# Kernel tuning notes

Measured on AMD Instinct MI355X. Metric: run time of the kernel, lower is better.

The kernel has to match this reference:

```python
import jax, jax.numpy as jnp
import numpy as np

F = 256

def setup_inputs() -> dict:
    key = jax.random.key(0)
    ks = jax.random.split(key, 6)
    s = 1.0 / np.sqrt(F)
    x = jax.random.normal(ks[0], (16, 1024, F), dtype=jnp.float32)
    W_alpha = jax.random.uniform(ks[1], (F, F), minval=-s, maxval=s, dtype=jnp.float32)
    W_beta = jax.random.uniform(ks[2], (F, F), minval=-s, maxval=s, dtype=jnp.float32)
    W_unary = jax.random.uniform(ks[3], (F, F), minval=-s, maxval=s, dtype=jnp.float32)
    b_unary = jax.random.uniform(ks[4], (F,), minval=-s, maxval=s, dtype=jnp.float32)
    W_r = jax.random.uniform(ks[5], (F, F), minval=-s, maxval=s, dtype=jnp.float32)
    return {"x": x, "W_alpha": W_alpha, "W_beta": W_beta, "W_unary": W_unary, "b_unary": b_unary, "W_r": W_r}

def reference(x, W_alpha, W_beta, W_unary, b_unary, W_r):
    # x: [B, N, F]; torch Linear computes x @ W^T (+ b)
    B, N, _ = x.shape
    alpha = jnp.einsum('bnf,gf->bng', x, W_alpha)
    beta = jnp.einsum('bnf,gf->bng', x, W_beta)
    unary = jnp.einsum('bnf,gf->bng', x, W_unary) + b_unary
    # scores: alpha_i . beta_j, diagonal excluded (i == j skipped in loop)
    scores = jnp.einsum('bif,bjf->bij', alpha, beta)
    scores = scores * (1.0 - jnp.eye(N, dtype=x.dtype))
    att = jnp.einsum('bij,bjf->bif', scores, unary) / N
    out = jnp.einsum('bif,gf->big', att, W_r) + x
    return out
```

## Files before the change

### kernel.cpp

```cpp
#include <hip/hip_runtime.h>


typedef __bf16 bf16;
typedef float floatx4 __attribute__((ext_vector_type(4)));
typedef bf16 bf16x8 __attribute__((ext_vector_type(8)));
typedef bf16 bf16x4 __attribute__((ext_vector_type(4)));

constexpr int FD = 256;
constexpr int NB = 16;
constexpr int NN = 1024;
constexpr int RR = NB * NN;

__global__ __launch_bounds__(256) void cvt_x(const float* __restrict__ x, bf16* __restrict__ xb) {
    int i = (blockIdx.x * 256 + threadIdx.x) * 4;
    float4 v = *(const float4*)&x[i];
    bf16x4 o = { (bf16)v.x, (bf16)v.y, (bf16)v.z, (bf16)v.w };
    *(bf16x4*)&xb[i] = o;
}

__global__ __launch_bounds__(256) void cvt_w(const float* Wa, const float* Wb, const float* Wu, const float* Wr,
                                             bf16* Wab, bf16* Wbb, bf16* Wub, bf16* Wrb) {
    const float* src; bf16* dst;
    switch (blockIdx.y) {
        case 0: src = Wa; dst = Wab; break;
        case 1: src = Wb; dst = Wbb; break;
        case 2: src = Wu; dst = Wub; break;
        default: src = Wr; dst = Wrb; break;
    }
    int i = (blockIdx.x * 256 + threadIdx.x) * 4;
    float4 v = *(const float4*)&src[i];
    bf16x4 o = { (bf16)v.x, (bf16)v.y, (bf16)v.z, (bf16)v.w };
    *(bf16x4*)&dst[i] = o;
}

__global__ __launch_bounds__(256)
void proj_mfma(const bf16* __restrict__ A,
               const bf16* __restrict__ W0, const bf16* __restrict__ W1, const bf16* __restrict__ W2,
               bf16* __restrict__ O0, bf16* __restrict__ O1, bf16* __restrict__ O2,
               const float* __restrict__ bu)
{
    constexpr int BM = 128, BN = 64, BK = 32, LDK = 40;
    __shared__ bf16 As[BM][LDK];
    __shared__ bf16 Bs[3][BN][LDK];
    const int tid = threadIdx.x;
    const int wave = tid >> 6, lane = tid & 63;
    const int q = lane >> 4, l16 = lane & 15;
    const int bm = blockIdx.y * BM, bn = blockIdx.x * BN;
    const bf16* Wp[3] = { W0, W1, W2 };

    floatx4 acc[3][2][4] = {};

    for (int k0 = 0; k0 < FD; k0 += BK) {
        {
            int c = tid;
            int row = c >> 2, k8 = (c & 3) * 8;
            *(int4*)&As[row][k8] = *(const int4*)&A[(size_t)(bm + row) * FD + k0 + k8];
            c = tid + 256; row = c >> 2; k8 = (c & 3) * 8;
            *(int4*)&As[row][k8] = *(const int4*)&A[(size_t)(bm + row) * FD + k0 + k8];
        }
        #pragma unroll
        for (int w = 0; w < 3; w++) {
            int row = tid >> 2, k8 = (tid & 3) * 8;
            *(int4*)&Bs[w][row][k8] = *(const int4*)&Wp[w][(size_t)(bn + row) * FD + k0 + k8];
        }
        __syncthreads();
        bf16x8 af[2];
        #pragma unroll
        for (int mi = 0; mi < 2; mi++)
            af[mi] = *(const bf16x8*)&As[wave * 32 + mi * 16 + l16][q * 8];
        #pragma unroll
        for (int w = 0; w < 3; w++) {
            bf16x8 bq[4];
            #pragma unroll
            for (int nj = 0; nj < 4; nj++)
                bq[nj] = *(const bf16x8*)&Bs[w][nj * 16 + l16][q * 8];
            #pragma unroll
            for (int mi = 0; mi < 2; mi++)
                #pragma unroll
                for (int nj = 0; nj < 4; nj++)
                    acc[w][mi][nj] = __builtin_amdgcn_mfma_f32_16x16x32_bf16(af[mi], bq[nj], acc[w][mi][nj], 0, 0, 0);
        }
        __syncthreads();
    }

    bf16* Op[3] = { O0, O1, O2 };
    #pragma unroll
    for (int w = 0; w < 3; w++) {
        #pragma unroll
        for (int mi = 0; mi < 2; mi++)
            #pragma unroll
            for (int i = 0; i < 4; i++) {
                int m = bm + wave * 32 + mi * 16 + q * 4 + i;
                #pragma unroll
                for (int nj = 0; nj < 4; nj++) {
                    int n = bn + nj * 16 + l16;
                    float v = acc[w][mi][nj][i];
                    if (w == 2) v += bu[n];
                    Op[w][(size_t)m * FD + n] = (bf16)v;
                }
            }
    }
}

template<int MODE>
__global__ __launch_bounds__(256)
void gemm_nt_mfma(const bf16* __restrict__ A, const bf16* __restrict__ Bmat, void* __restrict__ Cout,
                  const float* __restrict__ dvec, const bf16* __restrict__ U,
                  const float* __restrict__ res, int batchB)
{
    constexpr int BM = 128, BN = 64, BK = 32, LDK = 40;
    __shared__ bf16 As[BM][LDK];
    __shared__ bf16 Bs[BN][LDK];
    const int tid = threadIdx.x;
    const int wave = tid >> 6, lane = tid & 63;
    const int q = lane >> 4, l16 = lane & 15;
    const int bm = blockIdx.y * BM, bn = blockIdx.x * BN;
    const bf16* Bp = Bmat + (batchB ? (size_t)(bm >> 10) * FD * FD : 0);

    floatx4 acc[2][4] = {};

    for (int k0 = 0; k0 < FD; k0 += BK) {
        {
            int c = tid;
            int row = c >> 2, k8 = (c & 3) * 8;
            *(int4*)&As[row][k8] = *(const int4*)&A[(size_t)(bm + row) * FD + k0 + k8];
            c = tid + 256; row = c >> 2; k8 = (c & 3) * 8;
            *(int4*)&As[row][k8] = *(const int4*)&A[(size_t)(bm + row) * FD + k0 + k8];
            int rb = tid >> 2, kb8 = (tid & 3) * 8;
            *(int4*)&Bs[rb][kb8] = *(const int4*)&Bp[(size_t)(bn + rb) * FD + k0 + kb8];
        }
        __syncthreads();
        bf16x8 af[2], bq[4];
        #pragma unroll
        for (int mi = 0; mi < 2; mi++)
            af[mi] = *(const bf16x8*)&As[wave * 32 + mi * 16 + l16][q * 8];
        #pragma unroll
        for (int nj = 0; nj < 4; nj++)
            bq[nj] = *(const bf16x8*)&Bs[nj * 16 + l16][q * 8];
        #pragma unroll
        for (int mi = 0; mi < 2; mi++)
            #pragma unroll
            for (int nj = 0; nj < 4; nj++)
                acc[mi][nj] = __builtin_amdgcn_mfma_f32_16x16x32_bf16(af[mi], bq[nj], acc[mi][nj], 0, 0, 0);
        __syncthreads();
    }

    #pragma unroll
    for (int mi = 0; mi < 2; mi++)
        #pragma unroll
        for (int i = 0; i < 4; i++) {
            int m = bm + wave * 32 + mi * 16 + q * 4 + i;
            float dm = (MODE == 2) ? dvec[m] : 0.0f;
            #pragma unroll
            for (int nj = 0; nj < 4; nj++) {
                int n = bn + nj * 16 + l16;
                float v = acc[mi][nj][i];
                if (MODE == 2) {
                    v = (v - dm * (float)U[(size_t)m * FD + n]) * (1.0f / 1024.0f);
                    ((bf16*)Cout)[(size_t)m * FD + n] = (bf16)v;
                } else if (MODE == 3) {
                    ((float*)Cout)[(size_t)m * FD + n] = v + res[(size_t)m * FD + n];
                } else {
                    ((bf16*)Cout)[(size_t)m * FD + n] = (bf16)v;
                }
            }
        }
}

__global__ __launch_bounds__(256)
void gemm_tn_mfma(const bf16* __restrict__ Uall, const bf16* __restrict__ Ball, float* __restrict__ Mpart)
{
    constexpr int BG = 64, BF = 64, BK = 32, LDK = 40, CHUNK = 256;
    __shared__ bf16 Ags[BG][LDK];
    __shared__ bf16 Bfs[BF][LDK];
    const int tid = threadIdx.x;
    const int wave = tid >> 6, lane = tid & 63;
    const int q = lane >> 4, l16 = lane & 15;
    const int b = blockIdx.z >> 2, chunk = blockIdx.z & 3;
    const int bg = blockIdx.y * BG, bfo = blockIdx.x * BF;
    const bf16* Ub = Uall + (size_t)b * NN * FD;
    const bf16* Bt = Ball + (size_t)b * NN * FD;

    floatx4 acc[4] = {};

    const int n0base = chunk * CHUNK;
    for (int nc = 0; nc < CHUNK; nc += BK) {
        {
            int nr = tid >> 3, g8 = (tid & 7) * 8;
            bf16x8 va = *(const bf16x8*)&Ub[(size_t)(n0base + nc + nr) * FD + bg + g8];
            bf16x8 vb = *(const bf16x8*)&Bt[(size_t)(n0base + nc + nr) * FD + bfo + g8];
            #pragma unroll
            for (int j = 0; j < 8; j++) {
                Ags[g8 + j][nr] = va[j];
                Bfs[g8 + j][nr] = vb[j];
            }
        }
        __syncthreads();
        bf16x8 af = *(const bf16x8*)&Ags[wave * 16 + l16][q * 8];
        #pragma unroll
        for (int fj = 0; fj < 4; fj++) {
            bf16x8 bq = *(const bf16x8*)&Bfs[fj * 16 + l16][q * 8];
            acc[fj] = __builtin_amdgcn_mfma_f32_16x16x32_bf16(af, bq, acc[fj], 0, 0, 0);
        }
        __syncthreads();
    }

    float* P = Mpart + (size_t)chunk * (NB * FD * FD) + (size_t)b * FD * FD;
    #pragma unroll
    for (int i = 0; i < 4; i++) {
        int g = bg + wave * 16 + q * 4 + i;
        #pragma unroll
        for (int fj = 0; fj < 4; fj++) {
            int f = bfo + fj * 16 + l16;
            P[(size_t)g * FD + f] = acc[fj][i];
        }
    }
}

__global__ __launch_bounds__(256) void reduce_M(const float* __restrict__ Mpart, bf16* __restrict__ Mt) {
    int i = (blockIdx.x * 256 + threadIdx.x) * 4;
    const size_t S = (size_t)NB * FD * FD;
    float4 a = *(const float4*)&Mpart[i];
    float4 c = *(const float4*)&Mpart[S + i];
    float4 e = *(const float4*)&Mpart[2 * S + i];
    float4 g = *(const float4*)&Mpart[3 * S + i];
    bf16x4 o = { (bf16)(a.x + c.x + e.x + g.x), (bf16)(a.y + c.y + e.y + g.y),
                 (bf16)(a.z + c.z + e.z + g.z), (bf16)(a.w + c.w + e.w + g.w) };
    *(bf16x4*)&Mt[i] = o;
}

__global__ __launch_bounds__(256)
void d_dot(const bf16* __restrict__ alpha, const bf16* __restrict__ beta, float* __restrict__ d) {
    const int row = blockIdx.x * 4 + (threadIdx.x >> 6);
    const int lane = threadIdx.x & 63;
    const size_t base = (size_t)row * FD;
    bf16x4 av = *(const bf16x4*)&alpha[base + lane * 4];
    bf16x4 bv = *(const bf16x4*)&beta[base + lane * 4];
    float s = (float)av[0] * (float)bv[0] + (float)av[1] * (float)bv[1] +
              (float)av[2] * (float)bv[2] + (float)av[3] * (float)bv[3];
    #pragma unroll
    for (int off = 32; off; off >>= 1) s += __shfl_xor(s, off);
    if (lane == 0) d[row] = s;
}

extern "C" void kernel_launch(void* const* d_in, const int* in_sizes, int n_in,
                              void* d_out, int out_size, void* d_ws, size_t ws_size,
                              hipStream_t stream)
{
    const float* x  = (const float*)d_in[0];
    const float* Wa = (const float*)d_in[1];
    const float* Wb = (const float*)d_in[2];
    const float* Wu = (const float*)d_in[3];
    const float* bu = (const float*)d_in[4];
    const float* Wr = (const float*)d_in[5];
    float* out = (float*)d_out;

    char* w = (char*)d_ws;
    bf16* xb    = (bf16*)w;                 w += (size_t)RR * FD * 2;
    bf16* Wab   = (bf16*)w;                 w += (size_t)FD * FD * 2;
    bf16* Wbb   = (bf16*)w;                 w += (size_t)FD * FD * 2;
    bf16* Wub   = (bf16*)w;                 w += (size_t)FD * FD * 2;
    bf16* Wrb   = (bf16*)w;                 w += (size_t)FD * FD * 2;
    bf16* alpha = (bf16*)w;                 w += (size_t)RR * FD * 2;
    bf16* beta  = (bf16*)w;                 w += (size_t)RR * FD * 2;
    bf16* unary = (bf16*)w;                 w += (size_t)RR * FD * 2;
    bf16* Tb    = (bf16*)w;                 w += (size_t)RR * FD * 2;
    float* dv   = (float*)w;                w += (size_t)RR * 4;
    float* Mpart= (float*)w;                w += (size_t)4 * NB * FD * FD * 4;
    bf16* Mt    = (bf16*)w;                 w += (size_t)NB * FD * FD * 2;

    dim3 blk(256);

    cvt_x<<<dim3(RR * FD / 1024), blk, 0, stream>>>(x, xb);
    cvt_w<<<dim3(FD * FD / 1024, 4), blk, 0, stream>>>(Wa, Wb, Wu, Wr, Wab, Wbb, Wub, Wrb);

    proj_mfma<<<dim3(FD / 64, RR / 128), blk, 0, stream>>>(xb, Wab, Wbb, Wub, alpha, beta, unary, bu);

    d_dot<<<dim3(RR / 4), blk, 0, stream>>>(alpha, beta, dv);

    gemm_tn_mfma<<<dim3(FD / 64, FD / 64, NB * 4), blk, 0, stream>>>(unary, beta, Mpart);
    reduce_M<<<dim3(NB * FD * FD / 1024), blk, 0, stream>>>(Mpart, Mt);

    gemm_nt_mfma<2><<<dim3(FD / 64, RR / 128), blk, 0, stream>>>(alpha, Mt, Tb, dv, unary, nullptr, 1);

    gemm_nt_mfma<3><<<dim3(FD / 64, RR / 128), blk, 0, stream>>>(Tb, Wrb, out, nullptr, nullptr, x, 0);
}
```

Before: 150.8 us.

## Fold output projection into per-batch matrix and fuse diagonal dot into projection

Reassociates the computation so that W_r is folded into the per-batch (beta^T unary) matrix, giving one small batched GEMM (qt_mfma). This removes the separate full-size output GEMM and the intermediate T buffer. The unary projection is pre-multiplied by W_r as a fourth projection (Wc = W_r·W_u, plus bias Wr·bu) inside the projection kernel. The diagonal alpha·beta dot is computed from the projection accumulators, and the weight conversions are merged into a single prep kernel along with the partial-sum reduction folded into qt_mfma. This cuts several launches and one large GEMM pass over activations. The cost is an extra 256-wide projection, a serial scalar prep for the Wc product, and additional bf16 rounding from reassociation.

```diff
diff --git a/kernel.cpp b/kernel.cpp
--- a/kernel.cpp
+++ b/kernel.cpp
@@ -11,55 +11,78 @@
 constexpr int NN = 1024;
 constexpr int RR = NB * NN;
 
-__global__ __launch_bounds__(256) void cvt_x(const float* __restrict__ x, bf16* __restrict__ xb) {
-    int i = (blockIdx.x * 256 + threadIdx.x) * 4;
-    float4 v = *(const float4*)&x[i];
-    bf16x4 o = { (bf16)v.x, (bf16)v.y, (bf16)v.z, (bf16)v.w };
-    *(bf16x4*)&xb[i] = o;
-}
-
-__global__ __launch_bounds__(256) void cvt_w(const float* Wa, const float* Wb, const float* Wu, const float* Wr,
-                                             bf16* Wab, bf16* Wbb, bf16* Wub, bf16* Wrb) {
-    const float* src; bf16* dst;
-    switch (blockIdx.y) {
-        case 0: src = Wa; dst = Wab; break;
-        case 1: src = Wb; dst = Wbb; break;
-        case 2: src = Wu; dst = Wub; break;
-        default: src = Wr; dst = Wrb; break;
-    }
-    int i = (blockIdx.x * 256 + threadIdx.x) * 4;
-    float4 v = *(const float4*)&src[i];
-    bf16x4 o = { (bf16)v.x, (bf16)v.y, (bf16)v.z, (bf16)v.w };
-    *(bf16x4*)&dst[i] = o;
-}
-
-__global__ __launch_bounds__(256)
-void proj_mfma(const bf16* __restrict__ A,
-               const bf16* __restrict__ W0, const bf16* __restrict__ W1, const bf16* __restrict__ W2,
-               bf16* __restrict__ O0, bf16* __restrict__ O1, bf16* __restrict__ O2,
-               const float* __restrict__ bu)
+__global__ __launch_bounds__(256)
+void prep(const float* __restrict__ x, const float* __restrict__ Wa, const float* __restrict__ Wb,
+          const float* __restrict__ Wu, const float* __restrict__ bu, const float* __restrict__ Wr,
+          bf16* __restrict__ xb, bf16* __restrict__ Wab, bf16* __restrict__ Wbb,
+          bf16* __restrict__ Wub, bf16* __restrict__ Wrb, bf16* __restrict__ Wcb,
+          float* __restrict__ bc)
+{
+    const int blk = blockIdx.x, tid = threadIdx.x;
+    if (blk < 2048) {
+        size_t i = ((size_t)blk * 256 + tid) * 8;
+        float4 v0 = *(const float4*)&x[i];
+        float4 v1 = *(const float4*)&x[i + 4];
+        bf16x8 o = { (bf16)v0.x, (bf16)v0.y, (bf16)v0.z, (bf16)v0.w,
+                     (bf16)v1.x, (bf16)v1.y, (bf16)v1.z, (bf16)v1.w };
+        *(bf16x8*)&xb[i] = o;
+    } else if (blk < 2080) {
+        int rel = blk - 2048, w = rel >> 3, wb = rel & 7;
+        const float* src = (w == 0) ? Wa : (w == 1) ? Wb : (w == 2) ? Wu : Wr;
+        bf16* dst = (w == 0) ? Wab : (w == 1) ? Wbb : (w == 2) ? Wub : Wrb;
+        for (int it = 0; it < 8; it++) {
+            int i = wb * 8192 + it * 1024 + tid * 4;
+            float4 v = *(const float4*)&src[i];
+            bf16x4 o = { (bf16)v.x, (bf16)v.y, (bf16)v.z, (bf16)v.w };
+            *(bf16x4*)&dst[i] = o;
+        }
+    } else if (blk < 2144) {
+        int j0 = (blk - 2080) * 4;
+        float acc[4] = {};
+        for (int g = 0; g < FD; g++) {
+            float wu = Wu[g * FD + tid];
+            #pragma unroll
+            for (int jr = 0; jr < 4; jr++)
+                acc[jr] += Wr[(j0 + jr) * FD + g] * wu;
+        }
+        #pragma unroll
+        for (int jr = 0; jr < 4; jr++)
+            Wcb[(j0 + jr) * FD + tid] = (bf16)acc[jr];
+    } else {
+        float s = 0.0f;
+        for (int g = 0; g < FD; g++) s += Wr[tid * FD + g] * bu[g];
+        bc[tid] = s;
+    }
+}
+
+__global__ __launch_bounds__(256)
+void proj4(const bf16* __restrict__ A,
+           const bf16* __restrict__ W0, const bf16* __restrict__ W1,
+           const bf16* __restrict__ W2, const bf16* __restrict__ W3,
+           bf16* __restrict__ O0, bf16* __restrict__ O1, bf16* __restrict__ O2, bf16* __restrict__ O3,
+           const float* __restrict__ bu, const float* __restrict__ bc,
+           float* __restrict__ dpart)
 {
     constexpr int BM = 128, BN = 64, BK = 32, LDK = 40;
     __shared__ bf16 As[BM][LDK];
-    __shared__ bf16 Bs[3][BN][LDK];
+    __shared__ bf16 Bs[4][BN][LDK];
     const int tid = threadIdx.x;
     const int wave = tid >> 6, lane = tid & 63;
     const int q = lane >> 4, l16 = lane & 15;
     const int bm = blockIdx.y * BM, bn = blockIdx.x * BN;
-    const bf16* Wp[3] = { W0, W1, W2 };
-
-    floatx4 acc[3][2][4] = {};
+    const bf16* Wp[4] = { W0, W1, W2, W3 };
+
+    floatx4 acc[4][2][4] = {};
 
     for (int k0 = 0; k0 < FD; k0 += BK) {
         {
-            int c = tid;
-            int row = c >> 2, k8 = (c & 3) * 8;
+            int c = tid, row = c >> 2, k8 = (c & 3) * 8;
             *(int4*)&As[row][k8] = *(const int4*)&A[(size_t)(bm + row) * FD + k0 + k8];
             c = tid + 256; row = c >> 2; k8 = (c & 3) * 8;
             *(int4*)&As[row][k8] = *(const int4*)&A[(size_t)(bm + row) * FD + k0 + k8];
         }
         #pragma unroll
-        for (int w = 0; w < 3; w++) {
+        for (int w = 0; w < 4; w++) {
             int row = tid >> 2, k8 = (tid & 3) * 8;
             *(int4*)&Bs[w][row][k8] = *(const int4*)&Wp[w][(size_t)(bn + row) * FD + k0 + k8];
         }
@@ -69,7 +92,7 @@
         for (int mi = 0; mi < 2; mi++)
             af[mi] = *(const bf16x8*)&As[wave * 32 + mi * 16 + l16][q * 8];
         #pragma unroll
-        for (int w = 0; w < 3; w++) {
+        for (int w = 0; w < 4; w++) {
             bf16x8 bq[4];
             #pragma unroll
             for (int nj = 0; nj < 4; nj++)
@@ -83,9 +106,9 @@
         __syncthreads();
     }
 
-    bf16* Op[3] = { O0, O1, O2 };
-    #pragma unroll
-    for (int w = 0; w < 3; w++) {
+    bf16* Op[4] = { O0, O1, O2, O3 };
+    #pragma unroll
+    for (int w = 0; w < 4; w++) {
         #pragma unroll
         for (int mi = 0; mi < 2; mi++)
             #pragma unroll
@@ -96,79 +119,31 @@
                     int n = bn + nj * 16 + l16;
                     float v = acc[w][mi][nj][i];
                     if (w == 2) v += bu[n];
+                    if (w == 3) v += bc[n];
                     Op[w][(size_t)m * FD + n] = (bf16)v;
                 }
             }
     }
-}
-
-template<int MODE>
-__global__ __launch_bounds__(256)
-void gemm_nt_mfma(const bf16* __restrict__ A, const bf16* __restrict__ Bmat, void* __restrict__ Cout,
-                  const float* __restrict__ dvec, const bf16* __restrict__ U,
-                  const float* __restrict__ res, int batchB)
-{
-    constexpr int BM = 128, BN = 64, BK = 32, LDK = 40;
-    __shared__ bf16 As[BM][LDK];
-    __shared__ bf16 Bs[BN][LDK];
-    const int tid = threadIdx.x;
-    const int wave = tid >> 6, lane = tid & 63;
-    const int q = lane >> 4, l16 = lane & 15;
-    const int bm = blockIdx.y * BM, bn = blockIdx.x * BN;
-    const bf16* Bp = Bmat + (batchB ? (size_t)(bm >> 10) * FD * FD : 0);
-
-    floatx4 acc[2][4] = {};
-
-    for (int k0 = 0; k0 < FD; k0 += BK) {
-        {
-            int c = tid;
-            int row = c >> 2, k8 = (c & 3) * 8;
-            *(int4*)&As[row][k8] = *(const int4*)&A[(size_t)(bm + row) * FD + k0 + k8];
-            c = tid + 256; row = c >> 2; k8 = (c & 3) * 8;
-            *(int4*)&As[row][k8] = *(const int4*)&A[(size_t)(bm + row) * FD + k0 + k8];
-            int rb = tid >> 2, kb8 = (tid & 3) * 8;
-            *(int4*)&Bs[rb][kb8] = *(const int4*)&Bp[(size_t)(bn + rb) * FD + k0 + kb8];
-        }
-        __syncthreads();
-        bf16x8 af[2], bq[4];
-        #pragma unroll
-        for (int mi = 0; mi < 2; mi++)
-            af[mi] = *(const bf16x8*)&As[wave * 32 + mi * 16 + l16][q * 8];
-        #pragma unroll
-        for (int nj = 0; nj < 4; nj++)
-            bq[nj] = *(const bf16x8*)&Bs[nj * 16 + l16][q * 8];
-        #pragma unroll
-        for (int mi = 0; mi < 2; mi++)
+
+    #pragma unroll
+    for (int mi = 0; mi < 2; mi++)
+        #pragma unroll
+        for (int i = 0; i < 4; i++) {
+            float p = 0.0f;
             #pragma unroll
             for (int nj = 0; nj < 4; nj++)
-                acc[mi][nj] = __builtin_amdgcn_mfma_f32_16x16x32_bf16(af[mi], bq[nj], acc[mi][nj], 0, 0, 0);
-        __syncthreads();
-    }
-
-    #pragma unroll
-    for (int mi = 0; mi < 2; mi++)
-        #pragma unroll
-        for (int i = 0; i < 4; i++) {
-            int m = bm + wave * 32 + mi * 16 + q * 4 + i;
-            float dm = (MODE == 2) ? dvec[m] : 0.0f;
-            #pragma unroll
-            for (int nj = 0; nj < 4; nj++) {
-                int n = bn + nj * 16 + l16;
-                float v = acc[mi][nj][i];
-                if (MODE == 2) {
-                    v = (v - dm * (float)U[(size_t)m * FD + n]) * (1.0f / 1024.0f);
-                    ((bf16*)Cout)[(size_t)m * FD + n] = (bf16)v;
-                } else if (MODE == 3) {
-                    ((float*)Cout)[(size_t)m * FD + n] = v + res[(size_t)m * FD + n];
-                } else {
-                    ((bf16*)Cout)[(size_t)m * FD + n] = (bf16)v;
-                }
+                p += acc[0][mi][nj][i] * acc[1][mi][nj][i];
+            #pragma unroll
+            for (int off = 1; off < 16; off <<= 1) p += __shfl_xor(p, off);
+            if (l16 == 0) {
+                int m = bm + wave * 32 + mi * 16 + q * 4 + i;
+                dpart[(size_t)blockIdx.x * RR + m] = p;
             }
         }
 }
 
 __global__ __launch_bounds__(256)
-void gemm_tn_mfma(const bf16* __restrict__ Uall, const bf16* __restrict__ Ball, float* __restrict__ Mpart)
+void gemm_tn_mfma(const bf16* __restrict__ Aall, const bf16* __restrict__ Ball, float* __restrict__ Mpart)
 {
     constexpr int BG = 64, BF = 64, BK = 32, LDK = 40, CHUNK = 256;
     __shared__ bf16 Ags[BG][LDK];
@@ -178,22 +153,19 @@
     const int q = lane >> 4, l16 = lane & 15;
     const int b = blockIdx.z >> 2, chunk = blockIdx.z & 3;
     const int bg = blockIdx.y * BG, bfo = blockIdx.x * BF;
-    const bf16* Ub = Uall + (size_t)b * NN * FD;
-    const bf16* Bt = Ball + (size_t)b * NN * FD;
+    const bf16* Ab = Aall + (size_t)b * NN * FD;
+    const bf16* Bb = Ball + (size_t)b * NN * FD;
 
     floatx4 acc[4] = {};
-
     const int n0base = chunk * CHUNK;
     for (int nc = 0; nc < CHUNK; nc += BK) {
-        {
-            int nr = tid >> 3, g8 = (tid & 7) * 8;
-            bf16x8 va = *(const bf16x8*)&Ub[(size_t)(n0base + nc + nr) * FD + bg + g8];
-            bf16x8 vb = *(const bf16x8*)&Bt[(size_t)(n0base + nc + nr) * FD + bfo + g8];
-            #pragma unroll
-            for (int j = 0; j < 8; j++) {
-                Ags[g8 + j][nr] = va[j];
-                Bfs[g8 + j][nr] = vb[j];
-            }
+        int nr = tid >> 3, g8 = (tid & 7) * 8;
+        bf16x8 va = *(const bf16x8*)&Ab[(size_t)(n0base + nc + nr) * FD + bg + g8];
+        bf16x8 vb = *(const bf16x8*)&Bb[(size_t)(n0base + nc + nr) * FD + bfo + g8];
+        #pragma unroll
+        for (int j = 0; j < 8; j++) {
+            Ags[g8 + j][nr] = va[j];
+            Bfs[g8 + j][nr] = vb[j];
         }
         __syncthreads();
         bf16x8 af = *(const bf16x8*)&Ags[wave * 16 + l16][q * 8];
@@ -204,43 +176,114 @@
         }
         __syncthreads();
     }
-
     float* P = Mpart + (size_t)chunk * (NB * FD * FD) + (size_t)b * FD * FD;
     #pragma unroll
     for (int i = 0; i < 4; i++) {
         int g = bg + wave * 16 + q * 4 + i;
         #pragma unroll
-        for (int fj = 0; fj < 4; fj++) {
-            int f = bfo + fj * 16 + l16;
-            P[(size_t)g * FD + f] = acc[fj][i];
-        }
-    }
-}
-
-__global__ __launch_bounds__(256) void reduce_M(const float* __restrict__ Mpart, bf16* __restrict__ Mt) {
-    int i = (blockIdx.x * 256 + threadIdx.x) * 4;
+        for (int fj = 0; fj < 4; fj++)
+            P[(size_t)g * FD + bfo + fj * 16 + l16] = acc[fj][i];
+    }
+}
+
+__global__ __launch_bounds__(256)
+void qt_mfma(const bf16* __restrict__ Wrb, const float* __restrict__ Mpart, bf16* __restrict__ Qt)
+{
+    constexpr int BJ = 64, BKT = 64, BK = 32, LDK = 40;
+    __shared__ bf16 As[BJ][LDK];
+    __shared__ bf16 Bs[BKT][LDK];
+    const int tid = threadIdx.x;
+    const int wave = tid >> 6, lane = tid & 63;
+    const int q = lane >> 4, l16 = lane & 15;
+    const int b = blockIdx.z;
+    const int bj = blockIdx.y * BJ, bk = blockIdx.x * BKT;
     const size_t S = (size_t)NB * FD * FD;
-    float4 a = *(const float4*)&Mpart[i];
-    float4 c = *(const float4*)&Mpart[S + i];
-    float4 e = *(const float4*)&Mpart[2 * S + i];
-    float4 g = *(const float4*)&Mpart[3 * S + i];
-    bf16x4 o = { (bf16)(a.x + c.x + e.x + g.x), (bf16)(a.y + c.y + e.y + g.y),
-                 (bf16)(a.z + c.z + e.z + g.z), (bf16)(a.w + c.w + e.w + g.w) };
-    *(bf16x4*)&Mt[i] = o;
-}
-
-__global__ __launch_bounds__(256)
-void d_dot(const bf16* __restrict__ alpha, const bf16* __restrict__ beta, float* __restrict__ d) {
-    const int row = blockIdx.x * 4 + (threadIdx.x >> 6);
-    const int lane = threadIdx.x & 63;
-    const size_t base = (size_t)row * FD;
-    bf16x4 av = *(const bf16x4*)&alpha[base + lane * 4];
-    bf16x4 bv = *(const bf16x4*)&beta[base + lane * 4];
-    float s = (float)av[0] * (float)bv[0] + (float)av[1] * (float)bv[1] +
-              (float)av[2] * (float)bv[2] + (float)av[3] * (float)bv[3];
-    #pragma unroll
-    for (int off = 32; off; off >>= 1) s += __shfl_xor(s, off);
-    if (lane == 0) d[row] = s;
+    const float* Mb = Mpart + (size_t)b * FD * FD;
+
+    floatx4 acc[4] = {};
+    for (int n0 = 0; n0 < FD; n0 += BK) {
+        int row = tid >> 2, n8 = (tid & 3) * 8;
+        *(int4*)&As[row][n8] = *(const int4*)&Wrb[(size_t)(bj + row) * FD + n0 + n8];
+        const float* base = &Mb[(size_t)(bk + row) * FD + n0 + n8];
+        float4 s0 = *(const float4*)&base[0]       , s1 = *(const float4*)&base[4];
+        float4 t0 = *(const float4*)&base[S]       , t1 = *(const float4*)&base[S + 4];
+        float4 u0 = *(const float4*)&base[2 * S]   , u1 = *(const float4*)&base[2 * S + 4];
+        float4 v0 = *(const float4*)&base[3 * S]   , v1 = *(const float4*)&base[3 * S + 4];
+        bf16x8 o = { (bf16)(s0.x + t0.x + u0.x + v0.x), (bf16)(s0.y + t0.y + u0.y + v0.y),
+                     (bf16)(s0.z + t0.z + u0.z + v0.z), (bf16)(s0.w + t0.w + u0.w + v0.w),
+                     (bf16)(s1.x + t1.x + u1.x + v1.x), (bf16)(s1.y + t1.y + u1.y + v1.y),
+                     (bf16)(s1.z + t1.z + u1.z + v1.z), (bf16)(s1.w + t1.w + u1.w + v1.w) };
+        *(bf16x8*)&Bs[row][n8] = o;
+        __syncthreads();
+        bf16x8 af = *(const bf16x8*)&As[wave * 16 + l16][q * 8];
+        #pragma unroll
+        for (int kj = 0; kj < 4; kj++) {
+            bf16x8 bq = *(const bf16x8*)&Bs[kj * 16 + l16][q * 8];
+            acc[kj] = __builtin_amdgcn_mfma_f32_16x16x32_bf16(af, bq, acc[kj], 0, 0, 0);
+        }
+        __syncthreads();
+    }
+    bf16* Qb = Qt + (size_t)b * FD * FD;
+    #pragma unroll
+    for (int i = 0; i < 4; i++) {
+        int j = bj + wave * 16 + q * 4 + i;
+        #pragma unroll
+        for (int kj = 0; kj < 4; kj++)
+            Qb[(size_t)j * FD + bk + kj * 16 + l16] = (bf16)acc[kj][i];
+    }
+}
+
+__global__ __launch_bounds__(256)
+void final_mfma(const bf16* __restrict__ alpha, const bf16* __restrict__ Qt,
+                const float* __restrict__ dpart, const bf16* __restrict__ U2,
+                const float* __restrict__ x, float* __restrict__ out)
+{
+    constexpr int BM = 128, BN = 64, BK = 32, LDK = 40;
+    __shared__ bf16 As[BM][LDK];
+    __shared__ bf16 Bs[BN][LDK];
+    const int tid = threadIdx.x;
+    const int wave = tid >> 6, lane = tid & 63;
+    const int q = lane >> 4, l16 = lane & 15;
+    const int bm = blockIdx.y * BM, bn = blockIdx.x * BN;
+    const bf16* Qb = Qt + (size_t)(bm >> 10) * FD * FD;
+
+    floatx4 acc[2][4] = {};
+    for (int k0 = 0; k0 < FD; k0 += BK) {
+        int c = tid, row = c >> 2, k8 = (c & 3) * 8;
+        *(int4*)&As[row][k8] = *(const int4*)&alpha[(size_t)(bm + row) * FD + k0 + k8];
+        c = tid + 256; row = c >> 2; k8 = (c & 3) * 8;
+        *(int4*)&As[row][k8] = *(const int4*)&alpha[(size_t)(bm + row) * FD + k0 + k8];
+        int rb = tid >> 2, kb8 = (tid & 3) * 8;
+        *(int4*)&Bs[rb][kb8] = *(const int4*)&Qb[(size_t)(bn + rb) * FD + k0 + kb8];
+        __syncthreads();
+        bf16x8 af[2], bq[4];
+        #pragma unroll
+        for (int mi = 0; mi < 2; mi++)
+            af[mi] = *(const bf16x8*)&As[wave * 32 + mi * 16 + l16][q * 8];
+        #pragma unroll
+        for (int nj = 0; nj < 4; nj++)
+            bq[nj] = *(const bf16x8*)&Bs[nj * 16 + l16][q * 8];
+        #pragma unroll
+        for (int mi = 0; mi < 2; mi++)
+            #pragma unroll
+            for (int nj = 0; nj < 4; nj++)
+                acc[mi][nj] = __builtin_amdgcn_mfma_f32_16x16x32_bf16(af[mi], bq[nj], acc[mi][nj], 0, 0, 0);
+        __syncthreads();
+    }
+
+    #pragma unroll
+    for (int mi = 0; mi < 2; mi++)
+        #pragma unroll
+        for (int i = 0; i < 4; i++) {
+            int m = bm + wave * 32 + mi * 16 + q * 4 + i;
+            float d = dpart[m] + dpart[RR + m] + dpart[2 * RR + m] + dpart[3 * RR + m];
+            #pragma unroll
+            for (int nj = 0; nj < 4; nj++) {
+                int n = bn + nj * 16 + l16;
+                float v = (acc[mi][nj][i] - d * (float)U2[(size_t)m * FD + n]) * (1.0f / 1024.0f);
+                out[(size_t)m * FD + n] = v + x[(size_t)m * FD + n];
+            }
+        }
 }
 
 extern "C" void kernel_launch(void* const* d_in, const int* in_sizes, int n_in,
@@ -256,32 +299,31 @@
     float* out = (float*)d_out;
 
     char* w = (char*)d_ws;
-    bf16* xb    = (bf16*)w;                 w += (size_t)RR * FD * 2;
-    bf16* Wab   = (bf16*)w;                 w += (size_t)FD * FD * 2;
-    bf16* Wbb   = (bf16*)w;                 w += (size_t)FD * FD * 2;
-    bf16* Wub   = (bf16*)w;                 w += (size_t)FD * FD * 2;
-    bf16* Wrb   = (bf16*)w;                 w += (size_t)FD * FD * 2;
-    bf16* alpha = (bf16*)w;                 w += (size_t)RR * FD * 2;
-    bf16* beta  = (bf16*)w;                 w += (size_t)RR * FD * 2;
-    bf16* unary = (bf16*)w;                 w += (size_t)RR * FD * 2;
-    bf16* Tb    = (bf16*)w;                 w += (size_t)RR * FD * 2;
-    float* dv   = (float*)w;                w += (size_t)RR * 4;
-    float* Mpart= (float*)w;                w += (size_t)4 * NB * FD * FD * 4;
-    bf16* Mt    = (bf16*)w;                 w += (size_t)NB * FD * FD * 2;
+    bf16* xb    = (bf16*)w;  w += (size_t)RR * FD * 2;
+    bf16* Wab   = (bf16*)w;  w += (size_t)FD * FD * 2;
+    bf16* Wbb   = (bf16*)w;  w += (size_t)FD * FD * 2;
+    bf16* Wub   = (bf16*)w;  w += (size_t)FD * FD * 2;
+    bf16* Wrb   = (bf16*)w;  w += (size_t)FD * FD * 2;
+    bf16* Wcb   = (bf16*)w;  w += (size_t)FD * FD * 2;
+    float* bc   = (float*)w; w += (size_t)FD * 4;
+    bf16* alpha = (bf16*)w;  w += (size_t)RR * FD * 2;
+    bf16* beta  = (bf16*)w;  w += (size_t)RR * FD * 2;
+    bf16* unary = (bf16*)w;  w += (size_t)RR * FD * 2;
+    bf16* U2    = (bf16*)w;  w += (size_t)RR * FD * 2;
+    float* dpart= (float*)w; w += (size_t)4 * RR * 4;
+    float* Mpart= (float*)w; w += (size_t)4 * NB * FD * FD * 4;
+    bf16* Qt    = (bf16*)w;  w += (size_t)NB * FD * FD * 2;
 
     dim3 blk(256);
 
-    cvt_x<<<dim3(RR * FD / 1024), blk, 0, stream>>>(x, xb);
-    cvt_w<<<dim3(FD * FD / 1024, 4), blk, 0, stream>>>(Wa, Wb, Wu, Wr, Wab, Wbb, Wub, Wrb);
-
-    proj_mfma<<<dim3(FD / 64, RR / 128), blk, 0, stream>>>(xb, Wab, Wbb, Wub, alpha, beta, unary, bu);
-
-    d_dot<<<dim3(RR / 4), blk, 0, stream>>>(alpha, beta, dv);
-
-    gemm_tn_mfma<<<dim3(FD / 64, FD / 64, NB * 4), blk, 0, stream>>>(unary, beta, Mpart);
-    reduce_M<<<dim3(NB * FD * FD / 1024), blk, 0, stream>>>(Mpart, Mt);
-
-    gemm_nt_mfma<2><<<dim3(FD / 64, RR / 128), blk, 0, stream>>>(alpha, Mt, Tb, dv, unary, nullptr, 1);
-
-    gemm_nt_mfma<3><<<dim3(FD / 64, RR / 128), blk, 0, stream>>>(Tb, Wrb, out, nullptr, nullptr, x, 0);
-}
+    prep<<<dim3(2145), blk, 0, stream>>>(x, Wa, Wb, Wu, bu, Wr, xb, Wab, Wbb, Wub, Wrb, Wcb, bc);
+
+    proj4<<<dim3(FD / 64, RR / 128), blk, 0, stream>>>(xb, Wab, Wbb, Wub, Wcb,
+                                                       alpha, beta, unary, U2, bu, bc, dpart);
+
+    gemm_tn_mfma<<<dim3(FD / 64, FD / 64, NB * 4), blk, 0, stream>>>(beta, unary, Mpart);
+
+    qt_mfma<<<dim3(FD / 64, FD / 64, NB), blk, 0, stream>>>(Wrb, Mpart, Qt);
+
+    final_mfma<<<dim3(FD / 64, RR / 128), blk, 0, stream>>>(alpha, Qt, dpart, U2, x, out);
+}
```

Result: slower. 167.2 us (+10.9%).
